# Kernel tuning notes

Hardware: AMD Instinct MI355X
Metric: run time of the kernel (lower is better)

The kernel has to match this reference:

```python
import jax, jax.numpy as jnp
import numpy as np

N_NODES = 50000
N_EDGES = 800000
D_IN = 128
D_HID = 128
NUM_LAYERS = 3
NUM_GRAPHS = 50


def setup_inputs() -> dict:
    key = jax.random.key(0)
    ks = jax.random.split(key, 8)
    x = jax.random.normal(ks[0], (N_NODES, D_IN), dtype=jnp.float32)
    edge_index = jax.random.randint(ks[1], (2, N_EDGES), 0, N_NODES, dtype=jnp.int32)
    batch = jnp.sort(jax.random.randint(ks[2], (N_NODES,), 0, NUM_GRAPHS, dtype=jnp.int32))
    # glorot-ish init for GCN weights and fc weights
    scale = 1.0 / np.sqrt(D_HID)
    Wc = jax.random.normal(ks[3], (NUM_LAYERS, D_IN, D_HID), dtype=jnp.float32) * scale
    bc = jnp.zeros((NUM_LAYERS, D_HID), dtype=jnp.float32)
    Wf = jax.random.normal(ks[4], (NUM_LAYERS, D_HID, D_HID), dtype=jnp.float32) * scale
    bf = jnp.zeros((NUM_LAYERS, D_HID), dtype=jnp.float32)
    return {"x": x, "edge_index": edge_index, "batch": batch,
            "Wc": Wc, "bc": bc, "Wf": Wf, "bf": bf}


def _gcn_forward(x, Wc, bc, Wf, bf, src, dst, deg_inv_sqrt, batch):
    norm = deg_inv_sqrt[src] * deg_inv_sqrt[dst]  # [E+N]
    for i in range(NUM_LAYERS):
        h = x @ Wc[i]                              # [N, D_HID] linear transform
        msg = h[src] * norm[:, None]               # gather + normalize, [E+N, D_HID]
        x = jax.ops.segment_sum(msg, dst, num_segments=N_NODES) + bc[i]
        x = jax.nn.relu(x)
    x = jax.ops.segment_sum(x, batch, num_segments=NUM_GRAPHS)  # global_add_pool
    for i in range(NUM_LAYERS):
        x = jax.nn.relu(x @ Wf[i] + bf[i])
    return x  # [NUM_GRAPHS, D_HID]


def reference(x, edge_index, batch, Wc, bc, Wf, bf):
    # add self-loops (PyG GCNConv default) and compute symmetric normalization
    loops = jnp.arange(N_NODES, dtype=edge_index.dtype)
    src = jnp.concatenate([edge_index[0], loops])
    dst = jnp.concatenate([edge_index[1], loops])
    deg = jax.ops.segment_sum(jnp.ones_like(dst, dtype=x.dtype), dst,
                              num_segments=N_NODES)
    deg_inv_sqrt = jnp.where(deg > 0, jax.lax.rsqrt(jnp.maximum(deg, 1.0)), 0.0)
    return _gcn_forward(x, Wc, bc, Wf, bf, src, dst, deg_inv_sqrt, batch)
```

## Files before the change

kernel.cpp:

```cpp
#include <hip/hip_runtime.h>

#define N_NODES 50000
#define N_EDGES 800000
#define D 128
#define NGRAPH 50

typedef unsigned int uint32;
typedef unsigned short u16;
typedef __attribute__((ext_vector_type(8))) short short8;
typedef __attribute__((ext_vector_type(4))) float f32x4;

__device__ inline float bf_lo(uint32 u) { union { uint32 u; float f; } c; c.u = u << 16; return c.f; }
__device__ inline float bf_hi(uint32 u) { union { uint32 u; float f; } c; c.u = u & 0xffff0000u; return c.f; }
__device__ inline u16 f2bf(float f) {
  union { float f; uint32 u; } c; c.f = f;
  uint32 r = (c.u + 0x7fffu + ((c.u >> 16) & 1u)) >> 16;
  return (u16)r;
}

__global__ void k_init(int* __restrict__ deg, const float* __restrict__ Wc,
                       u16* __restrict__ WT, const int* __restrict__ batch,
                       int* __restrict__ gstart) {
  int i = blockIdx.x * 256 + threadIdx.x;
  if (i < N_NODES) deg[i] = 0;
  if (i < 3 * 128 * 128) {
    int layer = i >> 14, rem = i & 16383;
    int n = rem >> 7, k = rem & 127;
    WT[i] = f2bf(Wc[layer * 16384 + k * 128 + n]);
  }
  if (i <= NGRAPH) {
    int lo = 0, hi = N_NODES;
    while (lo < hi) {
      int mid = (lo + hi) >> 1;
      if (batch[mid] < i) lo = mid + 1; else hi = mid;
    }
    gstart[i] = lo;
  }
}

__global__ void k_degfill(const int* __restrict__ src, const int* __restrict__ dst,
                          int* __restrict__ deg, u16* __restrict__ csr) {
  int part = blockIdx.x & 7;
  int e = (blockIdx.x >> 3) * 256 + threadIdx.x;
  if (e < N_EDGES) {
    int d = dst[e];
    if (d / 6250 == part) {
      int r = atomicAdd(&deg[d], 1);
      csr[(d << 6) + r] = (u16)src[e];
    }
  }
}

template <int AF32>
__global__ __launch_bounds__(256) void k_gemm(const void* __restrict__ Ap,
                                              const u16* __restrict__ WT,
                                              const int* __restrict__ deg,
                                              u16* __restrict__ G) {
  __shared__ u16 so[4][16][136];
  int t = threadIdx.x;
  int wave = t >> 6, l = t & 63;
  int cl = l & 15, kgrp = l >> 4;
  int r0 = blockIdx.x * 64 + wave * 16;
  int arow = r0 + cl;
  bool valid = arow < N_NODES;

  const short8* B8 = reinterpret_cast<const short8*>(WT);

  f32x4 acc[8] = {};
#pragma unroll
  for (int k0 = 0; k0 < 4; ++k0) {
    short8 a = {};
    if (valid) {
      if (AF32) {
        const float4* A4 = reinterpret_cast<const float4*>(Ap);
        float4 v0 = A4[(size_t)arow * 32 + (k0 * 4 + kgrp) * 2];
        float4 v1 = A4[(size_t)arow * 32 + (k0 * 4 + kgrp) * 2 + 1];
        a[0] = (short)f2bf(v0.x); a[1] = (short)f2bf(v0.y);
        a[2] = (short)f2bf(v0.z); a[3] = (short)f2bf(v0.w);
        a[4] = (short)f2bf(v1.x); a[5] = (short)f2bf(v1.y);
        a[6] = (short)f2bf(v1.z); a[7] = (short)f2bf(v1.w);
      } else {
        a = reinterpret_cast<const short8*>(Ap)[(size_t)arow * 16 + k0 * 4 + kgrp];
      }
    }
#pragma unroll
    for (int c = 0; c < 8; ++c) {
      short8 b = B8[(c * 16 + cl) * 16 + k0 * 4 + kgrp];
      acc[c] = __builtin_amdgcn_mfma_f32_16x16x32_bf16(a, b, acc[c], 0, 0, 0);
    }
  }

  int rloc = kgrp * 4;
  float dj[4];
#pragma unroll
  for (int j = 0; j < 4; ++j) {
    int rr = r0 + rloc + j;
    dj[j] = (rr < N_NODES) ? rsqrtf((float)deg[rr] + 1.0f) : 0.f;
  }
#pragma unroll
  for (int c = 0; c < 8; ++c) {
#pragma unroll
    for (int j = 0; j < 4; ++j) {
      so[wave][rloc + j][c * 16 + cl] = f2bf(dj[j] * acc[c][j]);
    }
  }
#pragma unroll
  for (int i = 0; i < 4; ++i) {
    int idx = i * 64 + l;
    int rr = idx >> 4, ch = idx & 15;
    int grow = r0 + rr;
    if (grow < N_NODES) {
      *reinterpret_cast<uint4*>(&(((u16*)G)[(size_t)grow * 128 + ch * 8])) =
          *reinterpret_cast<const uint4*>(&so[wave][rr][ch * 8]);
    }
  }
}

#define ACCUM(u) do { \
    a0 += bf_lo((u).x); a1 += bf_hi((u).x); a2 += bf_lo((u).y); a3 += bf_hi((u).y); \
    a4 += bf_lo((u).z); a5 += bf_hi((u).z); a6 += bf_lo((u).w); a7 += bf_hi((u).w); } while (0)

template <int OUT_BF16>
__global__ __launch_bounds__(256) void k_agg(const uint4* __restrict__ g4,
                                             const int* __restrict__ deg,
                                             const u16* __restrict__ csr,
                                             const float* __restrict__ bc,
                                             void* __restrict__ xo) {
  int w = threadIdx.x >> 6;
  int i = blockIdx.x * 4 + w;
  if (i >= N_NODES) return;
  int l = threadIdx.x & 63;
  int q = l >> 4, c = l & 15;

  int cnt = deg[i];
  float di = rsqrtf((float)cnt + 1.0f);

  float a0 = 0.f, a1 = 0.f, a2 = 0.f, a3 = 0.f;
  float a4 = 0.f, a5 = 0.f, a6 = 0.f, a7 = 0.f;
  if (q == 0) {
    uint4 su = g4[(size_t)i * 16 + c];
    ACCUM(su);
  }

  int myidx = (l < cnt) ? (int)csr[(i << 6) + l] : 0;

  int nq = cnt >> 2;
  int j = 0;
  for (; j + 4 <= nq; j += 4) {
    int s0 = __shfl(myidx, 4 * j + q);
    int s1 = __shfl(myidx, 4 * j + 4 + q);
    int s2 = __shfl(myidx, 4 * j + 8 + q);
    int s3 = __shfl(myidx, 4 * j + 12 + q);
    uint4 u0 = g4[(size_t)s0 * 16 + c];
    uint4 u1 = g4[(size_t)s1 * 16 + c];
    uint4 u2 = g4[(size_t)s2 * 16 + c];
    uint4 u3 = g4[(size_t)s3 * 16 + c];
    ACCUM(u0); ACCUM(u1); ACCUM(u2); ACCUM(u3);
  }
  for (; j < nq; ++j) {
    int s = __shfl(myidx, 4 * j + q);
    uint4 u = g4[(size_t)s * 16 + c];
    ACCUM(u);
  }
  if (cnt & 3) {
    int idx = 4 * nq + q;
    int s = __shfl(myidx, idx < cnt ? idx : 0);
    if (idx < cnt) {
      uint4 u = g4[(size_t)s * 16 + c];
      ACCUM(u);
    }
  }
  a0 += __shfl_xor(a0, 16); a0 += __shfl_xor(a0, 32);
  a1 += __shfl_xor(a1, 16); a1 += __shfl_xor(a1, 32);
  a2 += __shfl_xor(a2, 16); a2 += __shfl_xor(a2, 32);
  a3 += __shfl_xor(a3, 16); a3 += __shfl_xor(a3, 32);
  a4 += __shfl_xor(a4, 16); a4 += __shfl_xor(a4, 32);
  a5 += __shfl_xor(a5, 16); a5 += __shfl_xor(a5, 32);
  a6 += __shfl_xor(a6, 16); a6 += __shfl_xor(a6, 32);
  a7 += __shfl_xor(a7, 16); a7 += __shfl_xor(a7, 32);

  if (q == 0) {
    float4 b0 = reinterpret_cast<const float4*>(bc)[c * 2];
    float4 b1 = reinterpret_cast<const float4*>(bc)[c * 2 + 1];
    float r0 = fmaxf(fmaf(di, a0, b0.x), 0.f);
    float r1 = fmaxf(fmaf(di, a1, b0.y), 0.f);
    float r2 = fmaxf(fmaf(di, a2, b0.z), 0.f);
    float r3 = fmaxf(fmaf(di, a3, b0.w), 0.f);
    float r4 = fmaxf(fmaf(di, a4, b1.x), 0.f);
    float r5 = fmaxf(fmaf(di, a5, b1.y), 0.f);
    float r6 = fmaxf(fmaf(di, a6, b1.z), 0.f);
    float r7 = fmaxf(fmaf(di, a7, b1.w), 0.f);
    if (OUT_BF16) {
      uint4 o;
      o.x = ((uint32)f2bf(r1) << 16) | f2bf(r0);
      o.y = ((uint32)f2bf(r3) << 16) | f2bf(r2);
      o.z = ((uint32)f2bf(r5) << 16) | f2bf(r4);
      o.w = ((uint32)f2bf(r7) << 16) | f2bf(r6);
      reinterpret_cast<uint4*>(xo)[(size_t)i * 16 + c] = o;
    } else {
      reinterpret_cast<float4*>(xo)[(size_t)i * 32 + c * 2] = make_float4(r0, r1, r2, r3);
      reinterpret_cast<float4*>(xo)[(size_t)i * 32 + c * 2 + 1] = make_float4(r4, r5, r6, r7);
    }
  }
}

__global__ __launch_bounds__(256) void k_pool(const float* __restrict__ x,
                                              const int* __restrict__ gstart,
                                              float* __restrict__ pp) {
  __shared__ float2 red[4][64];
  int g = blockIdx.x, ch = blockIdx.y;
  int s = gstart[g], e = gstart[g + 1];
  long len = e - s;
  int cs = s + (int)(len * ch / 8);
  int ce = s + (int)(len * (ch + 1) / 8);
  int sub = threadIdx.x >> 6, l = threadIdx.x & 63;
  const float2* x2 = reinterpret_cast<const float2*>(x);
  float2 acc = make_float2(0.f, 0.f);
  for (int n = cs + sub; n < ce; n += 4) {
    float2 v = x2[(size_t)n * 64 + l];
    acc.x += v.x;
    acc.y += v.y;
  }
  red[sub][l] = acc;
  __syncthreads();
  if (sub == 0) {
    float2 a = red[0][l];
    a.x += red[1][l].x + red[2][l].x + red[3][l].x;
    a.y += red[1][l].y + red[2][l].y + red[3][l].y;
    pp[(ch * NGRAPH + g) * D + 2 * l] = a.x;
    pp[(ch * NGRAPH + g) * D + 2 * l + 1] = a.y;
  }
}

__global__ __launch_bounds__(128) void k_fc(const float* __restrict__ pp,
                                            const float* __restrict__ Wf,
                                            const float* __restrict__ bf,
                                            float* __restrict__ out) {
  __shared__ float row[D];
  int g = blockIdx.x, c = threadIdx.x;
  float v = 0.f;
#pragma unroll
  for (int ch = 0; ch < 8; ++ch) v += pp[(ch * NGRAPH + g) * D + c];
  row[c] = v;
  __syncthreads();
  for (int l = 0; l < 3; ++l) {
    const float* W = Wf + l * D * D;
    float s = bf[l * D + c];
    for (int k = 0; k < D; ++k) s = fmaf(row[k], W[k * D + c], s);
    s = fmaxf(s, 0.f);
    __syncthreads();
    row[c] = s;
    __syncthreads();
  }
  out[g * D + c] = row[c];
}

extern "C" void kernel_launch(void* const* d_in, const int* in_sizes, int n_in,
                              void* d_out, int out_size, void* d_ws, size_t ws_size,
                              hipStream_t stream) {
  const float* x   = (const float*)d_in[0];
  const int*   ei  = (const int*)d_in[1];
  const int* batch = (const int*)d_in[2];
  const float* Wc  = (const float*)d_in[3];
  const float* bc  = (const float*)d_in[4];
  const float* Wf  = (const float*)d_in[5];
  const float* bf  = (const float*)d_in[6];
  float* out = (float*)d_out;
  const int* src = ei;
  const int* dst = ei + N_EDGES;

  char* ws = (char*)d_ws;
  size_t o = 0;
  auto take = [&](size_t b) -> void* {
    void* p = ws + o;
    o = (o + b + 255) & ~(size_t)255;
    return p;
  };
  int*  deg    = (int*)take(N_NODES * 4);
  int*  gstart = (int*)take(64 * 4);
  u16*  WT     = (u16*)take((size_t)3 * D * D * 2);
  u16*  csr    = (u16*)take((size_t)N_NODES * 64 * 2);
  u16*  xb     = (u16*)take((size_t)N_NODES * D * 2);
  u16*  gbuf   = (u16*)take((size_t)N_NODES * D * 2);
  float* xbuf  = (float*)take((size_t)N_NODES * D * 4);
  float* pp    = (float*)take((size_t)8 * NGRAPH * D * 4);
  (void)ws_size; (void)in_sizes; (void)n_in; (void)out_size;

  const int NB = (N_NODES + 255) / 256;
  k_init<<<NB, 256, 0, stream>>>(deg, Wc, WT, batch, gstart);
  k_degfill<<<8 * ((N_EDGES + 255) / 256), 256, 0, stream>>>(src, dst, deg, csr);

  const int GB = (N_NODES + 63) / 64;
  const int AB = (N_NODES + 3) / 4;
  k_gemm<1><<<GB, 256, 0, stream>>>(x, WT + 0 * D * D, deg, gbuf);
  k_agg<1><<<AB, 256, 0, stream>>>((const uint4*)gbuf, deg, csr, bc + 0 * D, xb);
  k_gemm<0><<<GB, 256, 0, stream>>>(xb, WT + 1 * D * D, deg, gbuf);
  k_agg<1><<<AB, 256, 0, stream>>>((const uint4*)gbuf, deg, csr, bc + 1 * D, xb);
  k_gemm<0><<<GB, 256, 0, stream>>>(xb, WT + 2 * D * D, deg, gbuf);
  k_agg<0><<<AB, 256, 0, stream>>>((const uint4*)gbuf, deg, csr, bc + 2 * D, xbuf);

  k_pool<<<dim3(NGRAPH, 8), 256, 0, stream>>>(xbuf, gstart, pp);
  k_fc<<<NGRAPH, 128, 0, stream>>>(pp, Wf, bf, out);
}
```

Measured before the change: 231.7 us.

## Split aggregation feature dim into four passes with 16 edges per wave step

The aggregation kernel now launches four times as many blocks, and each pass handles a 32-feature slice (64 bytes per row) instead of the full 128-feature row. Within a wave, 16 edge slots with 4 lanes each gather neighbours in parallel, so the edge list is walked in steps of 16 rather than 4. This exposes more independent gathers per step and more blocks to keep memory busy. In exchange, each row is fetched as 64-byte partial segments across passes, the CSR index load and degree read are repeated four times, and the cross-lane reduction gains two extra shuffle stages.

```diff
diff --git a/kernel.cpp b/kernel.cpp
--- a/kernel.cpp
+++ b/kernel.cpp
@@ -120,68 +120,56 @@
     a0 += bf_lo((u).x); a1 += bf_hi((u).x); a2 += bf_lo((u).y); a3 += bf_hi((u).y); \
     a4 += bf_lo((u).z); a5 += bf_hi((u).z); a6 += bf_lo((u).w); a7 += bf_hi((u).w); } while (0)
 
+#define NODE_BLOCKS ((N_NODES + 3) / 4)
+
 template <int OUT_BF16>
 __global__ __launch_bounds__(256) void k_agg(const uint4* __restrict__ g4,
                                              const int* __restrict__ deg,
                                              const u16* __restrict__ csr,
                                              const float* __restrict__ bc,
                                              void* __restrict__ xo) {
+  int pass = blockIdx.x / NODE_BLOCKS;
+  int nb = blockIdx.x % NODE_BLOCKS;
   int w = threadIdx.x >> 6;
-  int i = blockIdx.x * 4 + w;
+  int i = nb * 4 + w;
   if (i >= N_NODES) return;
   int l = threadIdx.x & 63;
-  int q = l >> 4, c = l & 15;
+  int eslot = l >> 2, cg = l & 3;
+  int p4 = pass * 4;
 
   int cnt = deg[i];
   float di = rsqrtf((float)cnt + 1.0f);
 
   float a0 = 0.f, a1 = 0.f, a2 = 0.f, a3 = 0.f;
   float a4 = 0.f, a5 = 0.f, a6 = 0.f, a7 = 0.f;
-  if (q == 0) {
-    uint4 su = g4[(size_t)i * 16 + c];
+  if (eslot == 0) {
+    uint4 su = g4[(size_t)i * 16 + p4 + cg];
     ACCUM(su);
   }
 
   int myidx = (l < cnt) ? (int)csr[(i << 6) + l] : 0;
 
-  int nq = cnt >> 2;
-  int j = 0;
-  for (; j + 4 <= nq; j += 4) {
-    int s0 = __shfl(myidx, 4 * j + q);
-    int s1 = __shfl(myidx, 4 * j + 4 + q);
-    int s2 = __shfl(myidx, 4 * j + 8 + q);
-    int s3 = __shfl(myidx, 4 * j + 12 + q);
-    uint4 u0 = g4[(size_t)s0 * 16 + c];
-    uint4 u1 = g4[(size_t)s1 * 16 + c];
-    uint4 u2 = g4[(size_t)s2 * 16 + c];
-    uint4 u3 = g4[(size_t)s3 * 16 + c];
-    ACCUM(u0); ACCUM(u1); ACCUM(u2); ACCUM(u3);
-  }
-  for (; j < nq; ++j) {
-    int s = __shfl(myidx, 4 * j + q);
-    uint4 u = g4[(size_t)s * 16 + c];
-    ACCUM(u);
-  }
-  if (cnt & 3) {
-    int idx = 4 * nq + q;
-    int s = __shfl(myidx, idx < cnt ? idx : 0);
-    if (idx < cnt) {
-      uint4 u = g4[(size_t)s * 16 + c];
-      ACCUM(u);
-    }
-  }
-  a0 += __shfl_xor(a0, 16); a0 += __shfl_xor(a0, 32);
-  a1 += __shfl_xor(a1, 16); a1 += __shfl_xor(a1, 32);
-  a2 += __shfl_xor(a2, 16); a2 += __shfl_xor(a2, 32);
-  a3 += __shfl_xor(a3, 16); a3 += __shfl_xor(a3, 32);
-  a4 += __shfl_xor(a4, 16); a4 += __shfl_xor(a4, 32);
-  a5 += __shfl_xor(a5, 16); a5 += __shfl_xor(a5, 32);
-  a6 += __shfl_xor(a6, 16); a6 += __shfl_xor(a6, 32);
-  a7 += __shfl_xor(a7, 16); a7 += __shfl_xor(a7, 32);
-
-  if (q == 0) {
-    float4 b0 = reinterpret_cast<const float4*>(bc)[c * 2];
-    float4 b1 = reinterpret_cast<const float4*>(bc)[c * 2 + 1];
+#pragma unroll 2
+  for (int j = 0; j < cnt; j += 16) {
+    int idx = j + eslot;
+    int ii = idx < cnt ? idx : 0;
+    int s = __shfl(myidx, ii);
+    uint4 u = g4[(size_t)s * 16 + p4 + cg];
+    if (idx < cnt) ACCUM(u);
+  }
+
+  a0 += __shfl_xor(a0, 4); a0 += __shfl_xor(a0, 8); a0 += __shfl_xor(a0, 16); a0 += __shfl_xor(a0, 32);
+  a1 += __shfl_xor(a1, 4); a1 += __shfl_xor(a1, 8); a1 += __shfl_xor(a1, 16); a1 += __shfl_xor(a1, 32);
+  a2 += __shfl_xor(a2, 4); a2 += __shfl_xor(a2, 8); a2 += __shfl_xor(a2, 16); a2 += __shfl_xor(a2, 32);
+  a3 += __shfl_xor(a3, 4); a3 += __shfl_xor(a3, 8); a3 += __shfl_xor(a3, 16); a3 += __shfl_xor(a3, 32);
+  a4 += __shfl_xor(a4, 4); a4 += __shfl_xor(a4, 8); a4 += __shfl_xor(a4, 16); a4 += __shfl_xor(a4, 32);
+  a5 += __shfl_xor(a5, 4); a5 += __shfl_xor(a5, 8); a5 += __shfl_xor(a5, 16); a5 += __shfl_xor(a5, 32);
+  a6 += __shfl_xor(a6, 4); a6 += __shfl_xor(a6, 8); a6 += __shfl_xor(a6, 16); a6 += __shfl_xor(a6, 32);
+  a7 += __shfl_xor(a7, 4); a7 += __shfl_xor(a7, 8); a7 += __shfl_xor(a7, 16); a7 += __shfl_xor(a7, 32);
+
+  if (l < 4) {
+    float4 b0 = reinterpret_cast<const float4*>(bc)[pass * 8 + cg * 2];
+    float4 b1 = reinterpret_cast<const float4*>(bc)[pass * 8 + cg * 2 + 1];
     float r0 = fmaxf(fmaf(di, a0, b0.x), 0.f);
     float r1 = fmaxf(fmaf(di, a1, b0.y), 0.f);
     float r2 = fmaxf(fmaf(di, a2, b0.z), 0.f);
@@ -196,10 +184,10 @@
       o.y = ((uint32)f2bf(r3) << 16) | f2bf(r2);
       o.z = ((uint32)f2bf(r5) << 16) | f2bf(r4);
       o.w = ((uint32)f2bf(r7) << 16) | f2bf(r6);
-      reinterpret_cast<uint4*>(xo)[(size_t)i * 16 + c] = o;
+      reinterpret_cast<uint4*>(xo)[(size_t)i * 16 + p4 + cg] = o;
     } else {
-      reinterpret_cast<float4*>(xo)[(size_t)i * 32 + c * 2] = make_float4(r0, r1, r2, r3);
-      reinterpret_cast<float4*>(xo)[(size_t)i * 32 + c * 2 + 1] = make_float4(r4, r5, r6, r7);
+      reinterpret_cast<float4*>(xo)[(size_t)i * 32 + (p4 + cg) * 2] = make_float4(r0, r1, r2, r3);
+      reinterpret_cast<float4*>(xo)[(size_t)i * 32 + (p4 + cg) * 2 + 1] = make_float4(r4, r5, r6, r7);
     }
   }
 }
@@ -291,7 +279,7 @@
   k_degfill<<<8 * ((N_EDGES + 255) / 256), 256, 0, stream>>>(src, dst, deg, csr);
 
   const int GB = (N_NODES + 63) / 64;
-  const int AB = (N_NODES + 3) / 4;
+  const int AB = 4 * NODE_BLOCKS;
   k_gemm<1><<<GB, 256, 0, stream>>>(x, WT + 0 * D * D, deg, gbuf);
   k_agg<1><<<AB, 256, 0, stream>>>((const uint4*)gbuf, deg, csr, bc + 0 * D, xb);
   k_gemm<0><<<GB, 256, 0, stream>>>(xb, WT + 1 * D * D, deg, gbuf);
```

After: 372.6 us. +60.8%, slower.
